# Optimization experiments

Hardware: AMD Instinct MI355X
Metric: run time of the kernel (lower is better)

Reference implementation:

```python
import jax, jax.numpy as jnp
import numpy as np

B, N, DIM = 2, 2048, 2048
N_HEAD, N_KV_HEAD = 32, 8
HEAD_DIM = DIM // N_HEAD  # 64
NEG_INF = -1e9


def setup_inputs() -> dict:
    key = jax.random.key(0)
    ks = jax.random.split(key, 4)
    x = jax.random.normal(ks[0], (B, N, DIM), dtype=jnp.float32)
    Wq = jax.random.normal(ks[1], (DIM, N_HEAD * HEAD_DIM), dtype=jnp.float32) * (DIM ** -0.5)
    Wkv = jax.random.normal(ks[2], (DIM, 2 * N_KV_HEAD * HEAD_DIM), dtype=jnp.float32) * (DIM ** -0.5)
    Wo = jax.random.normal(ks[3], (N_HEAD * HEAD_DIM, DIM), dtype=jnp.float32) * (DIM ** -0.5)
    # RoPE angles: freqs = 1/theta^(2i/d), angle[p, i] = p * freqs[i]
    freqs = 1.0 / (10000.0 ** (jnp.arange(0, HEAD_DIM, 2, dtype=jnp.float32) / HEAD_DIM))
    angles = jnp.arange(N, dtype=jnp.float32)[:, None] * freqs[None, :]  # (N, HEAD_DIM//2)
    rope_cos = jnp.cos(angles)
    rope_sin = jnp.sin(angles)
    # additive causal mask (n, n)
    mask = jnp.where(jnp.tril(jnp.ones((N, N), dtype=bool)), 0.0, NEG_INF).astype(jnp.float32)
    return {"x": x, "Wq": Wq, "Wkv": Wkv, "Wo": Wo, "rope_cos": rope_cos, "rope_sin": rope_sin, "mask": mask, "start_pos": 0}


def apply_rope(x, cos, sin):
    # x: (b, n, h, d); cos/sin: (n, d//2). Complex mult on interleaved pairs.
    xr = x.reshape(*x.shape[:-1], HEAD_DIM // 2, 2)
    xe, xo = xr[..., 0], xr[..., 1]
    c = cos[None, :, None, :]
    s = sin[None, :, None, :]
    yr = xe * c - xo * s
    yi = xe * s + xo * c
    return jnp.stack([yr, yi], axis=-1).reshape(x.shape)


def reference(x, Wq, Wkv, Wo, rope_cos, rope_sin, mask, start_pos):
    b, n, _ = x.shape
    q = (x @ Wq).reshape(b, n, N_HEAD, HEAD_DIM)
    kv = (x @ Wkv).reshape(b, n, 2, N_KV_HEAD, HEAD_DIM)
    k, v = kv[:, :, 0], kv[:, :, 1]
    q = apply_rope(q, rope_cos, rope_sin)
    k = apply_rope(k, rope_cos, rope_sin)
    # repeat kv heads: 'b n h d -> b n (r h) d'
    r = N_HEAD // N_KV_HEAD
    k = jnp.tile(k, (1, 1, r, 1))
    v = jnp.tile(v, (1, 1, r, 1))
    scale = HEAD_DIM ** -0.5
    attn = jnp.einsum('bnhd,bmhd->bhnm', q, k) * scale + mask[None, None]
    attn = jax.nn.softmax(attn, axis=-1)
    out = jnp.einsum('bhnm,bmhd->bnhd', attn, v).reshape(b, n, N_HEAD * HEAD_DIM)
    return out @ Wo
```

## Files before the change

kernel.cpp:

```cpp
#include <hip/hip_runtime.h>


#define BSZ  2
#define NSEQ 2048
#define DIMD 2048
#define NH   32
#define NKV  8
#define HD   64
#define TK   32

typedef __bf16 bf16x8 __attribute__((ext_vector_type(8)));
typedef __bf16 bf16x4 __attribute__((ext_vector_type(4)));
typedef __bf16 bf16x2 __attribute__((ext_vector_type(2)));
typedef float  floatx4 __attribute__((ext_vector_type(4)));

#define MFMA16(a, b, c) __builtin_amdgcn_mfma_f32_16x16x32_bf16(a, b, c, 0, 0, 0)

#define WAITV(n) asm volatile("s_waitcnt vmcnt(" #n ")" ::: "memory")

__device__ __forceinline__ void barrier_nodrain() {
    asm volatile("" ::: "memory");
    __builtin_amdgcn_sched_barrier(0);
    __builtin_amdgcn_s_barrier();
    __builtin_amdgcn_sched_barrier(0);
    asm volatile("" ::: "memory");
}

__device__ __forceinline__ void gload_lds16(const void* g, void* l) {
    __builtin_amdgcn_global_load_lds((const __attribute__((address_space(1))) void*)g,
                                     (__attribute__((address_space(3))) void*)l, 16, 0, 0);
}

__global__ void cvt_x_kernel(const float* __restrict__ in, __bf16* __restrict__ out, int n4) {
    int i = blockIdx.x * blockDim.x + threadIdx.x;
    if (i >= n4) return;
    float4 v = ((const float4*)in)[i];
    bf16x4 o;
    o[0] = (__bf16)v.x; o[1] = (__bf16)v.y; o[2] = (__bf16)v.z; o[3] = (__bf16)v.w;
    ((bf16x4*)out)[i] = o;
}

__global__ void transpose_cvt_kernel(const float* __restrict__ W, __bf16* __restrict__ Wt,
                                     int C, int K) {
    __shared__ float t[32][33];
    int c0 = blockIdx.x * 32, r0 = blockIdx.y * 32;
    int lx = threadIdx.x & 31, ly = threadIdx.x >> 5;
    for (int i = 0; i < 32; i += 8)
        t[ly + i][lx] = W[(size_t)(r0 + ly + i) * C + c0 + lx];
    __syncthreads();
    for (int i = 0; i < 32; i += 8)
        Wt[(size_t)(c0 + ly + i) * K + r0 + lx] = (__bf16)t[lx][ly + i];
}


#define MMAC(mh, nh)                                                           \
    {                                                                          \
        asm volatile("s_waitcnt lgkmcnt(0)" ::: "memory");                     \
        __builtin_amdgcn_sched_barrier(0);                                     \
        __builtin_amdgcn_s_setprio(1);                                         \
        _Pragma("unroll")                                                      \
        for (int il = 0; il < 4; ++il)                                         \
            _Pragma("unroll")                                                  \
            for (int jl = 0; jl < 2; ++jl)                                     \
                _Pragma("unroll")                                              \
                for (int ks = 0; ks < 2; ++ks)                                 \
                    acc[(mh) * 4 + il][(nh) * 2 + jl] =                        \
                        MFMA16(af[il][ks], bfr[jl][ks],                        \
                               acc[(mh) * 4 + il][(nh) * 2 + jl]);             \
        __builtin_amdgcn_s_setprio(0);                                         \
        barrier_nodrain();                                                     \
    }

__device__ __forceinline__ void gemm256_8ph(const __bf16* __restrict__ Ap,
                                            const __bf16* __restrict__ Bp,
                                            __bf16* As, __bf16* Bs,
                                            floatx4 (&acc)[8][4]) {
    int tid = threadIdx.x;
    int wave = tid >> 6, lane = tid & 63;
    int wm = wave >> 2, wn = wave & 3;
    int quad = lane >> 4, l16 = lane & 15;
    int swk = l16 & 7;

    int srcc = ((tid & 7) ^ ((tid >> 3) & 7)) << 3;
    int srow = tid >> 3;
    int wb = wave * 512;

    auto stage = [&](const __bf16* panel, __bf16* region, int kt) {
        gload_lds16(panel + (size_t)srow * DIMD + kt * 64 + srcc, region + wb);
        gload_lds16(panel + (size_t)(64 + srow) * DIMD + kt * 64 + srcc,
                    region + 4096 + wb);
    };

    bf16x8 af[4][2], bfr[2][2];
    auto rdA = [&](const __bf16* R) {
        #pragma unroll
        for (int il = 0; il < 4; ++il) {
            int rl = (2 * il + wm) * 16 + l16;
            #pragma unroll
            for (int ks = 0; ks < 2; ++ks)
                af[il][ks] = *(const bf16x8*)&R[rl * 64 + (((ks * 4 + quad) ^ swk) << 3)];
        }
    };
    auto rdB = [&](const __bf16* R) {
        #pragma unroll
        for (int jl = 0; jl < 2; ++jl) {
            int rl = (4 * jl + wn) * 16 + l16;
            #pragma unroll
            for (int ks = 0; ks < 2; ++ks)
                bfr[jl][ks] = *(const bf16x8*)&R[rl * 64 + (((ks * 4 + quad) ^ swk) << 3)];
        }
    };

    const __bf16* ApH1 = Ap + (size_t)128 * DIMD;
    const __bf16* BpH1 = Bp + (size_t)128 * DIMD;

    stage(Ap,   As + 0,    0);  stage(ApH1, As + 8192, 0);
    stage(Bp,   Bs + 0,    0);  stage(BpH1, Bs + 8192, 0);
    stage(Ap,   As + 16384, 1); stage(BpH1, Bs + 16384 + 8192, 1);

    #pragma unroll 2
    for (int t = 0; t < TK; ++t) {
        int b = t & 1;
        __bf16* Ab  = As + (b << 14);
        __bf16* Bb  = Bs + (b << 14);
        __bf16* Aob = As + ((b ^ 1) << 14);
        __bf16* Bob = Bs + ((b ^ 1) << 14);

        if (t < TK - 1) { WAITV(4); } else { WAITV(0); }
        barrier_nodrain();

        rdA(Ab);
        rdB(Bb);
        if (t + 1 < TK) stage(ApH1, Aob + 8192, t + 1);
        MMAC(0, 0);
        rdB(Bb + 8192);
        if (t + 1 < TK) stage(Bp, Bob, t + 1);
        MMAC(0, 1);
        rdA(Ab + 8192);
        if (t + 2 < TK) stage(Ap, Ab, t + 2);
        MMAC(1, 1);
        rdB(Bb);
        if (t + 2 < TK) stage(BpH1, Bb + 8192, t + 2);
        MMAC(1, 0);
    }
}

#define AROW(i) (((i) >> 2 << 7) + ((2 * ((i) & 3) + wm) << 4) + (quad << 2))
#define BCOL(j) (((j) >> 1 << 7) + ((4 * ((j) & 1) + wn) << 4) + l16)

__global__ __launch_bounds__(512, 2) void gemm_qkv_kernel(
    const __bf16* __restrict__ A, const __bf16* __restrict__ Bt,
    const float* __restrict__ cosb, const float* __restrict__ sinb,
    __bf16* __restrict__ Qo, __bf16* __restrict__ Ko, __bf16* __restrict__ Vo) {
    __shared__ __align__(16) __bf16 As[2 * 2 * 8192];
    __shared__ __align__(16) __bf16 Bs[2 * 2 * 8192];
    int p0 = blockIdx.x * 256;
    int t0 = blockIdx.y * 256;

    floatx4 acc[8][4] = {};
    gemm256_8ph(Bt + (size_t)p0 * DIMD, A + (size_t)t0 * DIMD, As, Bs, acc);

    int tid = threadIdx.x;
    int wave = tid >> 6, lane = tid & 63;
    int wm = wave >> 2, wn = wave & 3;
    int quad = lane >> 4, l16 = lane & 15;
    bool isQ = p0 < 2048;
    bool isV = p0 >= 2560;
    const float sc = isQ ? 0.18033688f : 1.0f;

    #pragma unroll
    for (int i = 0; i < 8; ++i) {
        int pp = p0 + AROW(i);
        int dq = pp & 63;
        #pragma unroll
        for (int j = 0; j < 4; ++j) {
            int t = t0 + BCOL(j);
            int b = t >> 11, n = t & 2047;
            float x0 = acc[i][j][0], x1 = acc[i][j][1];
            float x2 = acc[i][j][2], x3 = acc[i][j][3];
            if (!isV) {
                int d2 = dq >> 1;
                float2 cv = *(const float2*)(cosb + (size_t)n * 32 + d2);
                float2 sv = *(const float2*)(sinb + (size_t)n * 32 + d2);
                bf16x4 o;
                o[0] = (__bf16)((x0 * cv.x - x1 * sv.x) * sc);
                o[1] = (__bf16)((x0 * sv.x + x1 * cv.x) * sc);
                o[2] = (__bf16)((x2 * cv.y - x3 * sv.y) * sc);
                o[3] = (__bf16)((x2 * sv.y + x3 * cv.y) * sc);
                if (isQ) {
                    int h = pp >> 6;
                    *(bf16x4*)&Qo[((size_t)(b * NH + h) * NSEQ + n) * HD + dq] = o;
                } else {
                    int kvh = (pp - 2048) >> 6;
                    *(bf16x4*)&Ko[((size_t)(b * NKV + kvh) * NSEQ + n) * HD + dq] = o;
                }
            } else {
                int kvh = (pp - 2560) >> 6;
                size_t base = (size_t)(b * NKV + kvh) * HD;
                Vo[(base + dq + 0) * NSEQ + n] = (__bf16)x0;
                Vo[(base + dq + 1) * NSEQ + n] = (__bf16)x1;
                Vo[(base + dq + 2) * NSEQ + n] = (__bf16)x2;
                Vo[(base + dq + 3) * NSEQ + n] = (__bf16)x3;
            }
        }
    }
}

__global__ __launch_bounds__(512, 2) void gemm_out_kernel(
    const __bf16* __restrict__ A, const __bf16* __restrict__ Bt,
    float* __restrict__ C) {
    __shared__ __align__(16) __bf16 As[2 * 2 * 8192];
    __shared__ __align__(16) __bf16 Bs[2 * 2 * 8192];
    int n0 = blockIdx.x * 256;
    int m0 = blockIdx.y * 256;

    floatx4 acc[8][4] = {};
    gemm256_8ph(A + (size_t)m0 * DIMD, Bt + (size_t)n0 * DIMD, As, Bs, acc);

    int tid = threadIdx.x;
    int wave = tid >> 6, lane = tid & 63;
    int wm = wave >> 2, wn = wave & 3;
    int quad = lane >> 4, l16 = lane & 15;
    #pragma unroll
    for (int i = 0; i < 8; ++i) {
        int row = m0 + AROW(i);
        #pragma unroll
        for (int j = 0; j < 4; ++j) {
            int col = n0 + BCOL(j);
            float* Cp = C + (size_t)row * 2048 + col;
            Cp[0]    = acc[i][j][0];
            Cp[2048] = acc[i][j][1];
            Cp[4096] = acc[i][j][2];
            Cp[6144] = acc[i][j][3];
        }
    }
}

__global__ __launch_bounds__(256) void attn_kernel(
    const __bf16* __restrict__ Q, const __bf16* __restrict__ K,
    const __bf16* __restrict__ Vt, __bf16* __restrict__ O) {
    __shared__ __align__(16) __bf16 Kl[2][64 * 64];
    __shared__ __align__(16) __bf16 Vl[2][64 * 64];
    __shared__ __align__(16) __bf16 Pl[4][16 * 64];

    int tid = threadIdx.x;
    int wave = tid >> 6, lane = tid & 63;
    int quad = lane >> 4, l16 = lane & 15;
    int bk = blockIdx.x;
    int b = bk >> 3, kvh = bk & 7;
    int h = kvh + wave * 8;
    int qt = 63 - blockIdx.y;
    int q0 = qt * 32;

    const __bf16* Qbase = Q + ((size_t)(b * NH + h)) * NSEQ * HD;
    const __bf16* Kbase = K + ((size_t)(b * NKV + kvh)) * NSEQ * HD;
    const __bf16* Vbase = Vt + ((size_t)(b * NKV + kvh)) * HD * NSEQ;
    __bf16* P = &Pl[wave][0];
    int swk = (l16 & 7) << 3;
    int swp = l16 & 7;

    auto stage = [&](int kt, int bi) {
        for (int r = 0; r < 2; ++r) {
            int obase = r * 2048 + wave * 512;
            int o = obase + lane * 8;
            int row = o >> 6;
            int el = (o & 63) ^ ((row & 7) << 3);
            gload_lds16(Kbase + (size_t)kt * 4096 + row * 64 + el, &Kl[bi][obase]);
            gload_lds16(Vbase + (size_t)row * NSEQ + kt * 64 + el, &Vl[bi][obase]);
        }
    };

    bf16x8 ones;
    #pragma unroll
    for (int t = 0; t < 8; ++t) ones[t] = (__bf16)1.0f;

    bf16x8 qf[2][2];
    #pragma unroll
    for (int s = 0; s < 2; ++s) {
        int qrow = q0 + s * 16 + l16;
        qf[s][0] = *(const bf16x8*)(Qbase + (size_t)qrow * HD + quad * 8);
        qf[s][1] = *(const bf16x8*)(Qbase + (size_t)qrow * HD + 32 + quad * 8);
    }

    floatx4 oa[2][4] = {};
    floatx4 lacc[2] = {};
    int ktmax = (q0 + 31) >> 6;
    int pb = 0;
    stage(0, 0);

    for (int kt = 0; kt <= ktmax; ++kt) {
        __syncthreads();
        if (kt < ktmax) stage(kt + 1, pb ^ 1);

        bool diag = (kt == ktmax);
        bool half_tile = diag && !(q0 & 32);

        bf16x8 kf[4][2], vf[4][2];
        #pragma unroll
        for (int j = 0; j < 4; ++j) {
            int rr = (j * 16 + l16) * 64;
            kf[j][0] = *(const bf16x8*)&Kl[pb][rr + ((quad * 8) ^ swk)];
            kf[j][1] = *(const bf16x8*)&Kl[pb][rr + ((quad * 8 + 32) ^ swk)];
            vf[j][0] = *(const bf16x8*)&Vl[pb][rr + ((quad * 8) ^ swk)];
            vf[j][1] = *(const bf16x8*)&Vl[pb][rr + ((quad * 8 + 32) ^ swk)];
        }

        auto qkj = [&](int j, int s, int q_l) {
            floatx4 sv = {0.f, 0.f, 0.f, 0.f};
            sv = MFMA16(kf[j][0], qf[s][0], sv);
            sv = MFMA16(kf[j][1], qf[s][1], sv);
            bf16x4 pk;
            if (diag) {
                int kvb = kt * 64 + j * 16 + quad * 4;
                #pragma unroll
                for (int r = 0; r < 4; ++r) {
                    float p = __builtin_exp2f(sv[r]);
                    if (kvb + r > q_l) p = 0.0f;
                    pk[r] = (__bf16)p;
                }
            } else {
                #pragma unroll
                for (int r = 0; r < 4; ++r) pk[r] = (__bf16)__builtin_exp2f(sv[r]);
            }
            *(bf16x4*)&P[l16 * 64 + ((((j << 1) + (quad >> 1)) ^ swp) << 3) +
                         ((quad & 1) << 2)] = pk;
        };

        #pragma unroll
        for (int s = 0; s < 2; ++s) {
            int q_l = q0 + s * 16 + l16;
            qkj(0, s, q_l);
            qkj(1, s, q_l);
            if (!half_tile) { qkj(2, s, q_l); qkj(3, s, q_l); }

            bf16x8 p0 = *(const bf16x8*)&P[l16 * 64 + ((quad ^ swp) << 3)];
            lacc[s] = MFMA16(ones, p0, lacc[s]);
            #pragma unroll
            for (int j = 0; j < 4; ++j)
                oa[s][j] = MFMA16(vf[j][0], p0, oa[s][j]);
            if (!half_tile) {
                bf16x8 p1 = *(const bf16x8*)&P[l16 * 64 + (((4 + quad) ^ swp) << 3)];
                lacc[s] = MFMA16(ones, p1, lacc[s]);
                #pragma unroll
                for (int j = 0; j < 4; ++j)
                    oa[s][j] = MFMA16(vf[j][1], p1, oa[s][j]);
            }
        }
        pb ^= 1;
    }

    #pragma unroll
    for (int s = 0; s < 2; ++s) {
        float inv = 1.0f / lacc[s][0];
        int n = q0 + s * 16 + l16;
        __bf16* Op = O + ((size_t)(b * NSEQ + n)) * (NH * HD) + h * HD + quad * 4;
        #pragma unroll
        for (int j = 0; j < 4; ++j) {
            bf16x4 ov;
            #pragma unroll
            for (int r = 0; r < 4; ++r) ov[r] = (__bf16)(oa[s][j][r] * inv);
            *(bf16x4*)(Op + j * 16) = ov;
        }
    }
}

extern "C" void kernel_launch(void* const* d_in, const int* in_sizes, int n_in,
                              void* d_out, int out_size, void* d_ws, size_t ws_size,
                              hipStream_t stream) {
    const float* x   = (const float*)d_in[0];
    const float* Wq  = (const float*)d_in[1];
    const float* Wkv = (const float*)d_in[2];
    const float* Wo  = (const float*)d_in[3];
    const float* rc  = (const float*)d_in[4];
    const float* rs  = (const float*)d_in[5];
    float* out = (float*)d_out;
    char* ws = (char*)d_ws;

    __bf16* xb    = (__bf16*)(ws + 0);
    __bf16* wqkvt = (__bf16*)(ws + 16777216);
    __bf16* wot   = (__bf16*)(ws + 29360128);
    __bf16* Qb    = (__bf16*)(ws + 37748736);
    __bf16* Kb    = (__bf16*)(ws + 54525952);
    __bf16* Vtb   = (__bf16*)(ws + 58720256);
    __bf16* attnb = (__bf16*)(ws + 62914560);

    cvt_x_kernel<<<8192, 256, 0, stream>>>(x, xb, 2097152);
    transpose_cvt_kernel<<<dim3(64, 64), 256, 0, stream>>>(Wq, wqkvt, 2048, 2048);
    transpose_cvt_kernel<<<dim3(32, 64), 256, 0, stream>>>(Wkv, wqkvt + (size_t)2048 * 2048, 1024, 2048);
    transpose_cvt_kernel<<<dim3(64, 64), 256, 0, stream>>>(Wo, wot, 2048, 2048);

    gemm_qkv_kernel<<<dim3(12, 16), 512, 0, stream>>>(xb, wqkvt, rc, rs, Qb, Kb, Vtb);

    attn_kernel<<<dim3(16, 64), 256, 0, stream>>>(Qb, Kb, Vtb, attnb);

    gemm_out_kernel<<<dim3(8, 16), 512, 0, stream>>>(attnb, wot, out);
}
```

Baseline: 334.6 us.

## Rewrite attention with 32x32 MFMA, register-held P, and 512-thread blocks

The attention kernel moves from 16x16x32 MFMA to 32x32x16 MFMA. The probability fragment now goes straight from the QK accumulator into the PV operand through a cross-half lane shuffle, replacing the round trip through LDS. The row sum is accumulated in scalar registers rather than by an MFMA against a ones vector. Blocks grow to 8 waves covering two 32-row query tiles for four heads each, so every staged K/V tile is shared by twice as many waves. This removes LDS P traffic and the extra sum MFMAs, at the cost of more register pressure and a per-block causal imbalance between the two query tiles.

```diff
diff --git a/kernel.cpp b/kernel.cpp
--- a/kernel.cpp
+++ b/kernel.cpp
@@ -13,8 +13,11 @@
 typedef __bf16 bf16x4 __attribute__((ext_vector_type(4)));
 typedef __bf16 bf16x2 __attribute__((ext_vector_type(2)));
 typedef float  floatx4 __attribute__((ext_vector_type(4)));
+typedef float  floatx16 __attribute__((ext_vector_type(16)));
+typedef unsigned int uintx4 __attribute__((ext_vector_type(4)));
 
 #define MFMA16(a, b, c) __builtin_amdgcn_mfma_f32_16x16x32_bf16(a, b, c, 0, 0, 0)
+#define MFMA32(a, b, c) __builtin_amdgcn_mfma_f32_32x32x16_bf16(a, b, c, 0, 0, 0)
 
 #define WAITV(n) asm volatile("s_waitcnt vmcnt(" #n ")" ::: "memory")
 
@@ -29,6 +32,11 @@
 __device__ __forceinline__ void gload_lds16(const void* g, void* l) {
     __builtin_amdgcn_global_load_lds((const __attribute__((address_space(1))) void*)g,
                                      (__attribute__((address_space(3))) void*)l, 16, 0, 0);
+}
+
+__device__ __forceinline__ unsigned pk2(float a, float b) {
+    bf16x2 t; t[0] = (__bf16)a; t[1] = (__bf16)b;
+    return __builtin_bit_cast(unsigned, t);
 }
 
 __global__ void cvt_x_kernel(const float* __restrict__ in, __bf16* __restrict__ out, int n4) {
@@ -236,132 +244,119 @@
     }
 }
 
-__global__ __launch_bounds__(256) void attn_kernel(
+__global__ __launch_bounds__(512) void attn_kernel(
     const __bf16* __restrict__ Q, const __bf16* __restrict__ K,
     const __bf16* __restrict__ Vt, __bf16* __restrict__ O) {
     __shared__ __align__(16) __bf16 Kl[2][64 * 64];
     __shared__ __align__(16) __bf16 Vl[2][64 * 64];
-    __shared__ __align__(16) __bf16 Pl[4][16 * 64];
 
     int tid = threadIdx.x;
     int wave = tid >> 6, lane = tid & 63;
-    int quad = lane >> 4, l16 = lane & 15;
+    int l31 = lane & 31, hi = lane >> 5;
     int bk = blockIdx.x;
     int b = bk >> 3, kvh = bk & 7;
-    int h = kvh + wave * 8;
-    int qt = 63 - blockIdx.y;
-    int q0 = qt * 32;
+    int j = 31 - (int)blockIdx.y;
+    int w01 = wave & 1;
+    int h = kvh + 8 * (wave >> 1);
+    int q0 = (2 * j + w01) * 32;
 
     const __bf16* Qbase = Q + ((size_t)(b * NH + h)) * NSEQ * HD;
     const __bf16* Kbase = K + ((size_t)(b * NKV + kvh)) * NSEQ * HD;
     const __bf16* Vbase = Vt + ((size_t)(b * NKV + kvh)) * HD * NSEQ;
-    __bf16* P = &Pl[wave][0];
-    int swk = (l16 & 7) << 3;
-    int swp = l16 & 7;
+    int swl = (l31 & 7) << 3;
 
     auto stage = [&](int kt, int bi) {
-        for (int r = 0; r < 2; ++r) {
-            int obase = r * 2048 + wave * 512;
-            int o = obase + lane * 8;
-            int row = o >> 6;
-            int el = (o & 63) ^ ((row & 7) << 3);
-            gload_lds16(Kbase + (size_t)kt * 4096 + row * 64 + el, &Kl[bi][obase]);
-            gload_lds16(Vbase + (size_t)row * NSEQ + kt * 64 + el, &Vl[bi][obase]);
-        }
+        int row = tid >> 3;
+        int el = ((tid & 7) << 3) ^ ((row & 7) << 3);
+        gload_lds16(Kbase + (size_t)kt * 4096 + row * 64 + el, &Kl[bi][wave * 512]);
+        gload_lds16(Vbase + (size_t)row * NSEQ + kt * 64 + el, &Vl[bi][wave * 512]);
     };
 
-    bf16x8 ones;
+    bf16x8 qf[4];
     #pragma unroll
-    for (int t = 0; t < 8; ++t) ones[t] = (__bf16)1.0f;
-
-    bf16x8 qf[2][2];
-    #pragma unroll
-    for (int s = 0; s < 2; ++s) {
-        int qrow = q0 + s * 16 + l16;
-        qf[s][0] = *(const bf16x8*)(Qbase + (size_t)qrow * HD + quad * 8);
-        qf[s][1] = *(const bf16x8*)(Qbase + (size_t)qrow * HD + 32 + quad * 8);
-    }
-
-    floatx4 oa[2][4] = {};
-    floatx4 lacc[2] = {};
-    int ktmax = (q0 + 31) >> 6;
+    for (int t = 0; t < 4; ++t)
+        qf[t] = *(const bf16x8*)(Qbase + (size_t)(q0 + l31) * HD + t * 16 + hi * 8);
+
+    floatx16 oacc[2] = {};
+    float lsum = 0.0f;
     int pb = 0;
     stage(0, 0);
 
-    for (int kt = 0; kt <= ktmax; ++kt) {
+    for (int kt = 0; kt <= j; ++kt) {
         __syncthreads();
-        if (kt < ktmax) stage(kt + 1, pb ^ 1);
-
-        bool diag = (kt == ktmax);
-        bool half_tile = diag && !(q0 & 32);
-
-        bf16x8 kf[4][2], vf[4][2];
-        #pragma unroll
-        for (int j = 0; j < 4; ++j) {
-            int rr = (j * 16 + l16) * 64;
-            kf[j][0] = *(const bf16x8*)&Kl[pb][rr + ((quad * 8) ^ swk)];
-            kf[j][1] = *(const bf16x8*)&Kl[pb][rr + ((quad * 8 + 32) ^ swk)];
-            vf[j][0] = *(const bf16x8*)&Vl[pb][rr + ((quad * 8) ^ swk)];
-            vf[j][1] = *(const bf16x8*)&Vl[pb][rr + ((quad * 8 + 32) ^ swk)];
-        }
-
-        auto qkj = [&](int j, int s, int q_l) {
-            floatx4 sv = {0.f, 0.f, 0.f, 0.f};
-            sv = MFMA16(kf[j][0], qf[s][0], sv);
-            sv = MFMA16(kf[j][1], qf[s][1], sv);
-            bf16x4 pk;
-            if (diag) {
-                int kvb = kt * 64 + j * 16 + quad * 4;
+        if (kt < j) stage(kt + 1, pb ^ 1);
+        const __bf16* Kp = &Kl[pb][0];
+        const __bf16* Vp = &Vl[pb][0];
+        bool diag = (kt == j);
+
+        #pragma unroll
+        for (int kvt = 0; kvt < 2; ++kvt) {
+            if (diag && !w01 && kvt == 1) continue;
+            bool domask = diag && (kvt == w01);
+
+            floatx16 s = {};
+            #pragma unroll
+            for (int t = 0; t < 4; ++t) {
+                bf16x8 ka = *(const bf16x8*)&Kp[(kvt * 32 + l31) * 64 +
+                                                ((t * 16 + hi * 8) ^ swl)];
+                s = MFMA32(ka, qf[t], s);
+            }
+
+            #pragma unroll
+            for (int ks = 0; ks < 2; ++ks) {
+                float e[8];
+                if (domask) {
+                    int q_l = q0 + l31;
+                    #pragma unroll
+                    for (int r = 0; r < 8; ++r) {
+                        int kv = kt * 64 + kvt * 32 + ks * 16 +
+                                 (r & 3) + 8 * (r >> 2) + 4 * hi;
+                        float p = __builtin_exp2f(s[ks * 8 + r]);
+                        e[r] = (kv > q_l) ? 0.0f : p;
+                    }
+                } else {
+                    #pragma unroll
+                    for (int r = 0; r < 8; ++r)
+                        e[r] = __builtin_exp2f(s[ks * 8 + r]);
+                }
                 #pragma unroll
-                for (int r = 0; r < 4; ++r) {
-                    float p = __builtin_exp2f(sv[r]);
-                    if (kvb + r > q_l) p = 0.0f;
-                    pk[r] = (__bf16)p;
+                for (int r = 0; r < 8; ++r) lsum += e[r];
+
+                unsigned a0 = pk2(e[0], e[1]), a1 = pk2(e[2], e[3]);
+                unsigned b0 = pk2(e[4], e[5]), b1 = pk2(e[6], e[7]);
+                unsigned t0 = hi ? a0 : b0, t1 = hi ? a1 : b1;
+                unsigned s0 = (unsigned)__shfl_xor((int)t0, 32, 64);
+                unsigned s1 = (unsigned)__shfl_xor((int)t1, 32, 64);
+                uintx4 fw;
+                fw[0] = hi ? s0 : a0;
+                fw[1] = hi ? s1 : a1;
+                fw[2] = hi ? b0 : s0;
+                fw[3] = hi ? b1 : s1;
+                bf16x8 pfrag = __builtin_bit_cast(bf16x8, fw);
+
+                #pragma unroll
+                for (int dt = 0; dt < 2; ++dt) {
+                    bf16x8 va = *(const bf16x8*)&Vp[(dt * 32 + l31) * 64 +
+                                    ((kvt * 32 + ks * 16 + hi * 8) ^ swl)];
+                    oacc[dt] = MFMA32(va, pfrag, oacc[dt]);
                 }
-            } else {
-                #pragma unroll
-                for (int r = 0; r < 4; ++r) pk[r] = (__bf16)__builtin_exp2f(sv[r]);
             }
-            *(bf16x4*)&P[l16 * 64 + ((((j << 1) + (quad >> 1)) ^ swp) << 3) +
-                         ((quad & 1) << 2)] = pk;
-        };
-
-        #pragma unroll
-        for (int s = 0; s < 2; ++s) {
-            int q_l = q0 + s * 16 + l16;
-            qkj(0, s, q_l);
-            qkj(1, s, q_l);
-            if (!half_tile) { qkj(2, s, q_l); qkj(3, s, q_l); }
-
-            bf16x8 p0 = *(const bf16x8*)&P[l16 * 64 + ((quad ^ swp) << 3)];
-            lacc[s] = MFMA16(ones, p0, lacc[s]);
-            #pragma unroll
-            for (int j = 0; j < 4; ++j)
-                oa[s][j] = MFMA16(vf[j][0], p0, oa[s][j]);
-            if (!half_tile) {
-                bf16x8 p1 = *(const bf16x8*)&P[l16 * 64 + (((4 + quad) ^ swp) << 3)];
-                lacc[s] = MFMA16(ones, p1, lacc[s]);
-                #pragma unroll
-                for (int j = 0; j < 4; ++j)
-                    oa[s][j] = MFMA16(vf[j][1], p1, oa[s][j]);
-            }
         }
         pb ^= 1;
     }
 
+    lsum += __shfl_xor(lsum, 32, 64);
+    float inv = 1.0f / lsum;
+    __bf16* Op = O + ((size_t)(b * NSEQ + q0 + l31)) * (NH * HD) + h * HD;
     #pragma unroll
-    for (int s = 0; s < 2; ++s) {
-        float inv = 1.0f / lacc[s][0];
-        int n = q0 + s * 16 + l16;
-        __bf16* Op = O + ((size_t)(b * NSEQ + n)) * (NH * HD) + h * HD + quad * 4;
-        #pragma unroll
-        for (int j = 0; j < 4; ++j) {
+    for (int dt = 0; dt < 2; ++dt)
+        #pragma unroll
+        for (int g = 0; g < 4; ++g) {
             bf16x4 ov;
             #pragma unroll
-            for (int r = 0; r < 4; ++r) ov[r] = (__bf16)(oa[s][j][r] * inv);
-            *(bf16x4*)(Op + j * 16) = ov;
-        }
-    }
+            for (int r = 0; r < 4; ++r) ov[r] = (__bf16)(oacc[dt][4 * g + r] * inv);
+            *(bf16x4*)(Op + dt * 32 + 8 * g + 4 * hi) = ov;
+        }
 }
 
 extern "C" void kernel_launch(void* const* d_in, const int* in_sizes, int n_in,
@@ -391,7 +386,7 @@
 
     gemm_qkv_kernel<<<dim3(12, 16), 512, 0, stream>>>(xb, wqkvt, rc, rs, Qb, Kb, Vtb);
 
-    attn_kernel<<<dim3(16, 64), 256, 0, stream>>>(Qb, Kb, Vtb, attnb);
+    attn_kernel<<<dim3(16, 32), 512, 0, stream>>>(Qb, Kb, Vtb, attnb);
 
     gemm_out_kernel<<<dim3(8, 16), 512, 0, stream>>>(attnb, wot, out);
 }
```

After: 340.3 us. No clear change (+1.7%).
